# Kernel tuning notes

Measured on AMD Instinct MI355X. Metric: run time of the kernel, lower is better.

## Reference

```python
import jax, jax.numpy as jnp
import numpy as np

N, X_DIM, Y_DIM, HID = 8192, 512, 2048 // 4, 2048
Y_DIM = 512

def setup_inputs() -> dict:
    key = jax.random.key(0)
    ks = jax.random.split(key, 10)
    def lin(k, fan_in, fan_out):
        lim = 1.0 / np.sqrt(fan_in)
        kw, kb = jax.random.split(k)
        W = jax.random.uniform(kw, (fan_in, fan_out), jnp.float32, -lim, lim)
        b = jax.random.uniform(kb, (fan_out,), jnp.float32, -lim, lim)
        return W, b
    mu_W1, mu_b1 = lin(ks[0], X_DIM, HID)
    mu_W2, mu_b2 = lin(ks[1], HID, Y_DIM)
    lv_W1, lv_b1 = lin(ks[2], X_DIM, HID)
    lv_W2, lv_b2 = lin(ks[3], HID, Y_DIM)
    return {
        "x_samples": jax.random.normal(ks[4], (N, X_DIM), jnp.float32),
        "y_samples": jax.random.normal(ks[5], (N, Y_DIM), jnp.float32),
        "mu_W1": mu_W1, "mu_b1": mu_b1, "mu_W2": mu_W2, "mu_b2": mu_b2,
        "lv_W1": lv_W1, "lv_b1": lv_b1, "lv_W2": lv_W2, "lv_b2": lv_b2,
    }

def reference(x_samples, y_samples, mu_W1, mu_b1, mu_W2, mu_b2, lv_W1, lv_b1, lv_W2, lv_b2):
    # MLP heads (GEMMs)
    mu = jax.nn.relu(x_samples @ mu_W1 + mu_b1) @ mu_W2 + mu_b2          # [N, D]
    logvar = jnp.tanh(jax.nn.relu(x_samples @ lv_W1 + lv_b1) @ lv_W2 + lv_b2)  # [N, D]
    w = 0.5 * jnp.exp(-logvar)                                           # 1/(2*exp(logvar))
    n = x_samples.shape[0]

    # positive: -mean_i sum_d (mu_id - y_id)^2 * w_id
    positive = -(((mu - y_samples) ** 2) * w).sum(axis=1).mean()

    # negative (exact decomposition of the [N,N,D] broadcast):
    # -(1/N^2) sum_{i,d} w_id * (N*mu_id^2 - 2*mu_id*Sy_d + Sy2_d)
    Sy = y_samples.sum(axis=0)          # [D]
    Sy2 = (y_samples ** 2).sum(axis=0)  # [D]
    negative = -(w * (n * mu ** 2 - 2.0 * mu * Sy + Sy2)).sum() / (n * n)

    return positive - negative
```

## Files before the change

kernel.cpp:

```cpp
#include <hip/hip_runtime.h>
#include <hip/hip_bf16.h>
#include <stdint.h>

#define NS   8192
#define XD   512
#define HD   2048
#define YD   512

typedef unsigned short u16;
using bf16x8 = __attribute__((ext_vector_type(8))) short;
using f32x4  = __attribute__((ext_vector_type(4))) float;

__device__ __forceinline__ float bf2f(u16 u) {
  union { uint32_t i; float f; } v; v.i = ((uint32_t)u) << 16; return v.f;
}
__device__ __forceinline__ u16 f2b(float f) {
  __hip_bfloat16 hb = __float2bfloat16(f);
  return *(const u16*)&hb;
}
__device__ __forceinline__ float ld_in(const void* p, int f32, size_t i) {
  return f32 ? ((const float*)p)[i] : bf2f(((const u16*)p)[i]);
}
#define GLDS(gp, lp) __builtin_amdgcn_global_load_lds( \
    (__attribute__((address_space(1))) void*)(gp),     \
    (__attribute__((address_space(3))) void*)(lp), 16, 0, 0)

__device__ __forceinline__ int probe_f32(const void* p, int n_u16, int* sflag) {
  if (threadIdx.x == 0) *sflag = 0;
  __syncthreads();
  const u16* q = (const u16*)p;
  int wild = 0;
  for (int i = threadIdx.x; i < n_u16; i += blockDim.x) {
    float v = bf2f(q[i]);
    if (!(fabsf(v) <= 1000.0f)) wild = 1;
  }
  if (wild) *sflag = 1;
  __syncthreads();
  int r = *sflag;
  __syncthreads();
  return r;
}

__device__ __forceinline__ void transpose64(const void* in, u16* out,
                                            int R, int C, int f, int t,
                                            u16* tile ) {
  const int tid = threadIdx.x;
  const int nbx = C >> 6;
  const int c0 = (t % nbx) * 64, r0 = (t / nbx) * 64;
  const int r = tid >> 2, cc = (tid & 3) * 16;
  if (f) {
    const float4* s = (const float4*)((const float*)in + (size_t)(r0 + r) * C + c0 + cc);
#pragma unroll
    for (int k = 0; k < 4; ++k) {
      float4 v = s[k];
      tile[r * 72 + cc + k * 4 + 0] = f2b(v.x);
      tile[r * 72 + cc + k * 4 + 1] = f2b(v.y);
      tile[r * 72 + cc + k * 4 + 2] = f2b(v.z);
      tile[r * 72 + cc + k * 4 + 3] = f2b(v.w);
    }
  } else {
    const uint4* s = (const uint4*)((const u16*)in + (size_t)(r0 + r) * C + c0 + cc);
    *(uint4*)&tile[r * 72 + cc]     = s[0];
    *(uint4*)&tile[r * 72 + cc + 8] = s[1];
  }
  __syncthreads();
  const int i = tid >> 2, jc = (tid & 3) * 16;
  alignas(16) u16 o[16];
#pragma unroll
  for (int j = 0; j < 16; ++j) o[j] = tile[(jc + j) * 72 + i];
  uint4* dq = (uint4*)&out[(size_t)(c0 + i) * R + r0 + jc];
  dq[0] = ((const uint4*)o)[0];
  dq[1] = ((const uint4*)o)[1];
}

__global__ __launch_bounds__(256) void prep_all(
    const void* __restrict__ x, const void* __restrict__ y,
    const void* w1m, const void* b1m, const void* w2m, const void* b2m,
    const void* w1l, const void* b1l, const void* w2l, const void* b2l,
    u16* __restrict__ xb, float* __restrict__ biasv,
    float* __restrict__ Sy, float* __restrict__ Sy2,
    u16* __restrict__ W1t, u16* __restrict__ W2tm, u16* __restrict__ W2tl,
    double* __restrict__ gacc, unsigned* __restrict__ counter) {
  __shared__ alignas(16) u16 tile[64 * 72];
  __shared__ int sflag;
  const int b = blockIdx.x;
  const int tid = threadIdx.x;

  if (b < 64) {
    const int yf = probe_f32(y, 1024, &sflag);
    const int c0 = b * 8;
    float s[8] = {}, q[8] = {};
    if (yf) {
      const float* fy = (const float*)y + c0;
      for (int r = tid; r < NS; r += 256) {
        const float4 a = *(const float4*)(fy + (size_t)r * YD);
        const float4 c = *(const float4*)(fy + (size_t)r * YD + 4);
        s[0]+=a.x; q[0]+=a.x*a.x; s[1]+=a.y; q[1]+=a.y*a.y;
        s[2]+=a.z; q[2]+=a.z*a.z; s[3]+=a.w; q[3]+=a.w*a.w;
        s[4]+=c.x; q[4]+=c.x*c.x; s[5]+=c.y; q[5]+=c.y*c.y;
        s[6]+=c.z; q[6]+=c.z*c.z; s[7]+=c.w; q[7]+=c.w*c.w;
      }
    } else {
      const u16* hy = (const u16*)y + c0;
      for (int r = tid; r < NS; r += 256) {
        const uint4 t4 = *(const uint4*)(hy + (size_t)r * YD);
        const uint32_t w4[4] = {t4.x, t4.y, t4.z, t4.w};
#pragma unroll
        for (int j = 0; j < 4; ++j) {
          const float v0 = bf2f((u16)(w4[j] & 0xffff));
          const float v1 = bf2f((u16)(w4[j] >> 16));
          s[2*j]   += v0; q[2*j]   += v0 * v0;
          s[2*j+1] += v1; q[2*j+1] += v1 * v1;
        }
      }
    }
    float* red = (float*)tile;
#pragma unroll
    for (int j = 0; j < 8; ++j) red[j * 256 + tid] = s[j];
    __syncthreads();
    for (int st = 128; st > 0; st >>= 1) {
      if (tid < st)
#pragma unroll
        for (int j = 0; j < 8; ++j) red[j * 256 + tid] += red[j * 256 + tid + st];
      __syncthreads();
    }
    if (tid < 8) Sy[c0 + tid] = red[tid * 256];
    __syncthreads();
#pragma unroll
    for (int j = 0; j < 8; ++j) red[j * 256 + tid] = q[j];
    __syncthreads();
    for (int st = 128; st > 0; st >>= 1) {
      if (tid < st)
#pragma unroll
        for (int j = 0; j < 8; ++j) red[j * 256 + tid] += red[j * 256 + tid + st];
      __syncthreads();
    }
    if (tid < 8) Sy2[c0 + tid] = red[tid * 256];
  } else if (b < 2112) {
    if (!probe_f32(x, 1024, &sflag)) return;
    const size_t base = (size_t)(b - 64) * 2048 + (size_t)tid * 8;
    alignas(16) u16 o[8];
    const float4* s = (const float4*)((const float*)x + base);
    float4 v0 = s[0], v1 = s[1];
    o[0]=f2b(v0.x); o[1]=f2b(v0.y); o[2]=f2b(v0.z); o[3]=f2b(v0.w);
    o[4]=f2b(v1.x); o[5]=f2b(v1.y); o[6]=f2b(v1.z); o[7]=f2b(v1.w);
    *(uint4*)(xb + base) = *(const uint4*)o;
  } else if (b == 2112) {
    if (tid == 0) { *gacc = 0.0; *counter = 0u; }
    const int f3 = probe_f32(b1m, 1024, &sflag);
    const int f5 = probe_f32(b2m, 512, &sflag);
    const int f7 = probe_f32(b1l, 1024, &sflag);
    const int f9 = probe_f32(b2l, 512, &sflag);
    for (int i = tid; i < 5120; i += 256) {
      float v;
      if (i < 2048)      v = ld_in(b1m, f3, i);
      else if (i < 4096) v = ld_in(b1l, f7, i - 2048);
      else if (i < 4608) v = ld_in(b2m, f5, i - 4096);
      else               v = ld_in(b2l, f9, i - 4608);
      biasv[i] = v;
    }
  } else {
    const int id = b - 2113, which = id >> 8, t = id & 255;
    const void* in; u16* out; int R, C;
    if (which == 0)      { in = w1m; out = W1t;                   R = XD; C = HD; }
    else if (which == 1) { in = w2m; out = W2tm;                  R = HD; C = YD; }
    else if (which == 2) { in = w1l; out = W1t + (size_t)HD * XD; R = XD; C = HD; }
    else                 { in = w2l; out = W2tl;                  R = HD; C = YD; }
    const int f = probe_f32(in, 1024, &sflag);
    transpose64(in, out, R, C, f, t, tile);
  }
}

__global__ __launch_bounds__(256) void gemm1_kernel(
    const void* __restrict__ xraw, const u16* __restrict__ xb,
    const u16* __restrict__ W1t,
    const float* __restrict__ bias,
    u16* __restrict__ h_mu, u16* __restrict__ h_lv) {
  constexpr int K = XD;
  __shared__ alignas(16) u16 As[128 * 64];
  __shared__ alignas(16) u16 Bs[128 * 64];
  __shared__ int sflag;

  const u16* A = probe_f32(xraw, 1024, &sflag) ? xb : (const u16*)xraw;

  const int tid = threadIdx.x, wid = tid >> 6, lane = tid & 63;
  const int MT = NS / 128, NT = (2 * HD) / 128;
  const int id = blockIdx.x;
  const int xcd = id & 7, slot = id >> 3;
  const int bm0 = (xcd * (MT >> 3) + slot / NT) * 128;
  const int bn0 = (slot % NT) * 128;

  const int mrow = (wid >> 1) * 64, ncol = (wid & 1) * 64;
  const int quad = lane >> 4, c16 = lane & 15, cswz = c16 & 7;
  const int srow = lane >> 3, sc = lane & 7;
  const int scg  = (sc ^ srow) * 8;

  f32x4 acc[4][4] = {};

  for (int k0 = 0; k0 < K; k0 += 64) {
#pragma unroll
    for (int j = 0; j < 4; ++j) {
      const int grp = wid * 4 + j, row = grp * 8 + srow;
      GLDS(A   + (size_t)(bm0 + row) * K + (k0 + scg), As + grp * 512);
      GLDS(W1t + (size_t)(bn0 + row) * K + (k0 + scg), Bs + grp * 512);
    }
    __syncthreads();
#pragma unroll
    for (int h = 0; h < 2; ++h) {
      const int off = ((h * 4 + quad) ^ cswz) * 8;
      bf16x8 af[4], bfr[4];
#pragma unroll
      for (int mi = 0; mi < 4; ++mi)
        af[mi] = *(const bf16x8*)&As[(mrow + mi * 16 + c16) * 64 + off];
#pragma unroll
      for (int ni = 0; ni < 4; ++ni)
        bfr[ni] = *(const bf16x8*)&Bs[(ncol + ni * 16 + c16) * 64 + off];
#pragma unroll
      for (int mi = 0; mi < 4; ++mi)
#pragma unroll
        for (int ni = 0; ni < 4; ++ni)
          acc[mi][ni] = __builtin_amdgcn_mfma_f32_16x16x32_bf16(
              af[mi], bfr[ni], acc[mi][ni], 0, 0, 0);
    }
    __syncthreads();
  }

  const bool is_lv = bn0 >= HD;
  u16* dst = is_lv ? h_lv : h_mu;
  const int cb = bn0 - (is_lv ? HD : 0);
#pragma unroll
  for (int ni = 0; ni < 4; ++ni) {
    const int gc = ncol + ni * 16 + c16;
    const float bv = bias[bn0 + gc];
#pragma unroll
    for (int mi = 0; mi < 4; ++mi)
#pragma unroll
      for (int r = 0; r < 4; ++r) {
        const int grow = bm0 + mrow + mi * 16 + quad * 4 + r;
        dst[(size_t)grow * HD + (cb + gc)] = f2b(fmaxf(acc[mi][ni][r] + bv, 0.f));
      }
  }
}

__global__ __launch_bounds__(256) void gemm2_dual(
    const u16* __restrict__ hm, const u16* __restrict__ hl,
    const u16* __restrict__ W2m, const u16* __restrict__ W2l,
    const float* __restrict__ b2m, const float* __restrict__ b2l,
    const void* __restrict__ y,
    const float* __restrict__ Sy, const float* __restrict__ Sy2,
    double* __restrict__ gacc, unsigned* __restrict__ counter,
    float* __restrict__ out) {
  constexpr int K = HD;
  __shared__ alignas(16) u16 Am[64 * 64];
  __shared__ alignas(16) u16 Al[64 * 64];
  __shared__ alignas(16) u16 Bm[128 * 64];
  __shared__ alignas(16) u16 Bl[128 * 64];
  __shared__ double bs[4];
  __shared__ int sflag;

  const int yf = probe_f32(y, 1024, &sflag);

  const int tid = threadIdx.x, wid = tid >> 6, lane = tid & 63;
  const int MT = NS / 64, NT = YD / 128;
  const int id = blockIdx.x;
  const int xcd = id & 7, slot = id >> 3;
  const int bm0 = (xcd * (MT >> 3) + slot / NT) * 64;
  const int bn0 = (slot % NT) * 128;

  const int mrow = (wid >> 1) * 32, ncol = (wid & 1) * 64;
  const int quad = lane >> 4, c16 = lane & 15, cswz = c16 & 7;
  const int srow = lane >> 3, sc = lane & 7;
  const int scg  = (sc ^ srow) * 8;

  f32x4 am[2][4] = {}, al[2][4] = {};

  for (int k0 = 0; k0 < K; k0 += 64) {
#pragma unroll
    for (int j = 0; j < 2; ++j) {
      const int grp = wid * 2 + j, row = grp * 8 + srow;
      const size_t go = (size_t)(bm0 + row) * K + (k0 + scg);
      GLDS(hm + go, Am + grp * 512);
      GLDS(hl + go, Al + grp * 512);
    }
#pragma unroll
    for (int j = 0; j < 4; ++j) {
      const int grp = wid * 4 + j, row = grp * 8 + srow;
      const size_t go = (size_t)(bn0 + row) * K + (k0 + scg);
      GLDS(W2m + go, Bm + grp * 512);
      GLDS(W2l + go, Bl + grp * 512);
    }
    __syncthreads();
#pragma unroll
    for (int h = 0; h < 2; ++h) {
      const int off = ((h * 4 + quad) ^ cswz) * 8;
      bf16x8 afm[2], afl[2], bfm[4], bfl[4];
#pragma unroll
      for (int mi = 0; mi < 2; ++mi) {
        const int rl = (mrow + mi * 16 + c16) * 64 + off;
        afm[mi] = *(const bf16x8*)&Am[rl];
        afl[mi] = *(const bf16x8*)&Al[rl];
      }
#pragma unroll
      for (int ni = 0; ni < 4; ++ni) {
        const int rl = (ncol + ni * 16 + c16) * 64 + off;
        bfm[ni] = *(const bf16x8*)&Bm[rl];
        bfl[ni] = *(const bf16x8*)&Bl[rl];
      }
#pragma unroll
      for (int mi = 0; mi < 2; ++mi)
#pragma unroll
        for (int ni = 0; ni < 4; ++ni) {
          am[mi][ni] = __builtin_amdgcn_mfma_f32_16x16x32_bf16(
              afm[mi], bfm[ni], am[mi][ni], 0, 0, 0);
          al[mi][ni] = __builtin_amdgcn_mfma_f32_16x16x32_bf16(
              afl[mi], bfl[ni], al[mi][ni], 0, 0, 0);
        }
    }
    __syncthreads();
  }

  const float invN = 1.0f / (float)NS;
  float s = 0.f;
#pragma unroll
  for (int ni = 0; ni < 4; ++ni) {
    const int gcol = bn0 + ncol + ni * 16 + c16;
    const float bmv = b2m[gcol], blv = b2l[gcol];
    const float syv = Sy[gcol], sy2v = Sy2[gcol];
#pragma unroll
    for (int mi = 0; mi < 2; ++mi)
#pragma unroll
      for (int r = 0; r < 4; ++r) {
        const int grow = bm0 + mrow + mi * 16 + quad * 4 + r;
        const float m   = am[mi][ni][r] + bmv;
        const float lvp = al[mi][ni][r] + blv;
        const float w   = 0.5f * expf(-tanhf(lvp));
        const float yv  = ld_in(y, yf, (size_t)grow * YD + gcol);
        s += w * (yv * yv - 2.f * m * yv + (2.f * m * syv - sy2v) * invN);
      }
  }
  for (int off = 32; off > 0; off >>= 1) s += __shfl_down(s, off);
  if (lane == 0) bs[wid] = (double)s;
  __syncthreads();
  if (tid == 0) {
    atomicAdd(gacc, bs[0] + bs[1] + bs[2] + bs[3]);
    __threadfence();
    const unsigned old = atomicAdd(counter, 1u);
    if (old == 511u) {
      const double g = atomicAdd(gacc, 0.0);
      out[0] = (float)(-g / (double)NS);
    }
  }
}

extern "C" void kernel_launch(void* const* d_in, const int* in_sizes, int n_in,
                              void* d_out, int out_size, void* d_ws, size_t ws_size,
                              hipStream_t stream) {
  char* ws = (char*)d_ws;
  double*   gacc    = (double*)ws;
  unsigned* counter = (unsigned*)(ws + 8);
  float*    Sy      = (float*)(ws + 128);
  float*    Sy2     = (float*)(ws + 2176);
  float*    biasv   = (float*)(ws + 4224);
  u16* xb   = (u16*)(ws + 24704);
  u16* W1t  = xb + (size_t)NS * XD;
  u16* W2tm = W1t + (size_t)2 * HD * XD;
  u16* W2tl = W2tm + (size_t)YD * HD;
  u16* h_mu = W2tl + (size_t)YD * HD;
  u16* h_lv = h_mu + (size_t)NS * HD;

  prep_all<<<3137, 256, 0, stream>>>(
      d_in[0], d_in[1], d_in[2], d_in[3], d_in[4], d_in[5],
      d_in[6], d_in[7], d_in[8], d_in[9],
      xb, biasv, Sy, Sy2, W1t, W2tm, W2tl, gacc, counter);

  const float* b1  = biasv;
  const float* b2m = biasv + 4096, *b2l = biasv + 4608;

  gemm1_kernel<<<(NS / 128) * ((2 * HD) / 128), 256, 0, stream>>>(
      d_in[0], xb, W1t, b1, h_mu, h_lv);

  gemm2_dual<<<(NS / 64) * (YD / 128), 256, 0, stream>>>(
      h_mu, h_lv, W2tm, W2tl, b2m, b2l, d_in[1], Sy, Sy2,
      gacc, counter, (float*)d_out);
}
```

Measured before the change: 232.2 us.

## Fuse prep and both GEMMs into one persistent cooperative kernel with grid syncs

Replaces the three kernel launches (prep, GEMM1, dual GEMM2) with a single cooperative persistent kernel. Blocks loop over work items and are separated by grid-wide syncs. It also moves all dtype probing to the kernel start and drops the completion counter in favour of a final grid sync. This is meant to remove launch gaps and tail effects between stages. In exchange, the grid size depends on occupancy, so the GEMM stages run with fewer resident blocks and the tile order changes. Every block also re-probes all ten inputs, and grid.sync adds its own cost.

```diff
diff --git a/kernel.cpp b/kernel.cpp
--- a/kernel.cpp
+++ b/kernel.cpp
@@ -1,6 +1,9 @@
 #include <hip/hip_runtime.h>
 #include <hip/hip_bf16.h>
+#include <hip/hip_cooperative_groups.h>
 #include <stdint.h>
+
+namespace cg = cooperative_groups;
 
 #define NS   8192
 #define XD   512
@@ -43,7 +46,7 @@
 
 __device__ __forceinline__ void transpose64(const void* in, u16* out,
                                             int R, int C, int f, int t,
-                                            u16* tile ) {
+                                            u16* tile) {
   const int tid = threadIdx.x;
   const int nbx = C >> 6;
   const int c0 = (t % nbx) * 64, r0 = (t / nbx) * 64;
@@ -73,294 +76,284 @@
   dq[1] = ((const uint4*)o)[1];
 }
 
-__global__ __launch_bounds__(256) void prep_all(
+__global__ __launch_bounds__(256, 3) void fused_all(
     const void* __restrict__ x, const void* __restrict__ y,
-    const void* w1m, const void* b1m, const void* w2m, const void* b2m,
-    const void* w1l, const void* b1l, const void* w2l, const void* b2l,
+    const void* __restrict__ w1m, const void* __restrict__ b1m,
+    const void* __restrict__ w2m, const void* __restrict__ b2m,
+    const void* __restrict__ w1l, const void* __restrict__ b1l,
+    const void* __restrict__ w2l, const void* __restrict__ b2l,
     u16* __restrict__ xb, float* __restrict__ biasv,
     float* __restrict__ Sy, float* __restrict__ Sy2,
     u16* __restrict__ W1t, u16* __restrict__ W2tm, u16* __restrict__ W2tl,
-    double* __restrict__ gacc, unsigned* __restrict__ counter) {
-  __shared__ alignas(16) u16 tile[64 * 72];
+    u16* __restrict__ h_mu, u16* __restrict__ h_lv,
+    double* __restrict__ gacc, float* __restrict__ out) {
+  __shared__ alignas(16) u16 smem[24576];
+  __shared__ double bs[4];
   __shared__ int sflag;
-  const int b = blockIdx.x;
   const int tid = threadIdx.x;
-
-  if (b < 64) {
-    const int yf = probe_f32(y, 1024, &sflag);
-    const int c0 = b * 8;
-    float s[8] = {}, q[8] = {};
-    if (yf) {
-      const float* fy = (const float*)y + c0;
-      for (int r = tid; r < NS; r += 256) {
-        const float4 a = *(const float4*)(fy + (size_t)r * YD);
-        const float4 c = *(const float4*)(fy + (size_t)r * YD + 4);
-        s[0]+=a.x; q[0]+=a.x*a.x; s[1]+=a.y; q[1]+=a.y*a.y;
-        s[2]+=a.z; q[2]+=a.z*a.z; s[3]+=a.w; q[3]+=a.w*a.w;
-        s[4]+=c.x; q[4]+=c.x*c.x; s[5]+=c.y; q[5]+=c.y*c.y;
-        s[6]+=c.z; q[6]+=c.z*c.z; s[7]+=c.w; q[7]+=c.w*c.w;
+  const int bid = blockIdx.x;
+  const int nblk = gridDim.x;
+
+  const int xf   = probe_f32(x,   1024, &sflag);
+  const int yf   = probe_f32(y,   1024, &sflag);
+  const int fw1m = probe_f32(w1m, 1024, &sflag);
+  const int fw2m = probe_f32(w2m, 1024, &sflag);
+  const int fw1l = probe_f32(w1l, 1024, &sflag);
+  const int fw2l = probe_f32(w2l, 1024, &sflag);
+  const int fb1m = probe_f32(b1m, 1024, &sflag);
+  const int fb2m = probe_f32(b2m, 512,  &sflag);
+  const int fb1l = probe_f32(b1l, 1024, &sflag);
+  const int fb2l = probe_f32(b2l, 512,  &sflag);
+
+  for (int w = bid; w < 3137; w += nblk) {
+    if (w < 64) {
+      const int c0 = w * 8;
+      float s[8] = {}, q[8] = {};
+      if (yf) {
+        const float* fy = (const float*)y + c0;
+        for (int r = tid; r < NS; r += 256) {
+          const float4 a = *(const float4*)(fy + (size_t)r * YD);
+          const float4 c = *(const float4*)(fy + (size_t)r * YD + 4);
+          s[0]+=a.x; q[0]+=a.x*a.x; s[1]+=a.y; q[1]+=a.y*a.y;
+          s[2]+=a.z; q[2]+=a.z*a.z; s[3]+=a.w; q[3]+=a.w*a.w;
+          s[4]+=c.x; q[4]+=c.x*c.x; s[5]+=c.y; q[5]+=c.y*c.y;
+          s[6]+=c.z; q[6]+=c.z*c.z; s[7]+=c.w; q[7]+=c.w*c.w;
+        }
+      } else {
+        const u16* hy = (const u16*)y + c0;
+        for (int r = tid; r < NS; r += 256) {
+          const uint4 t4 = *(const uint4*)(hy + (size_t)r * YD);
+          const uint32_t w4[4] = {t4.x, t4.y, t4.z, t4.w};
+#pragma unroll
+          for (int j = 0; j < 4; ++j) {
+            const float v0 = bf2f((u16)(w4[j] & 0xffff));
+            const float v1 = bf2f((u16)(w4[j] >> 16));
+            s[2*j]   += v0; q[2*j]   += v0 * v0;
+            s[2*j+1] += v1; q[2*j+1] += v1 * v1;
+          }
+        }
+      }
+      float* red = (float*)smem;
+#pragma unroll
+      for (int j = 0; j < 8; ++j) red[j * 256 + tid] = s[j];
+      __syncthreads();
+      for (int st = 128; st > 0; st >>= 1) {
+        if (tid < st)
+#pragma unroll
+          for (int j = 0; j < 8; ++j) red[j * 256 + tid] += red[j * 256 + tid + st];
+        __syncthreads();
+      }
+      if (tid < 8) Sy[c0 + tid] = red[tid * 256];
+      __syncthreads();
+#pragma unroll
+      for (int j = 0; j < 8; ++j) red[j * 256 + tid] = q[j];
+      __syncthreads();
+      for (int st = 128; st > 0; st >>= 1) {
+        if (tid < st)
+#pragma unroll
+          for (int j = 0; j < 8; ++j) red[j * 256 + tid] += red[j * 256 + tid + st];
+        __syncthreads();
+      }
+      if (tid < 8) Sy2[c0 + tid] = red[tid * 256];
+    } else if (w < 2112) {
+      if (xf) {
+        const size_t base = (size_t)(w - 64) * 2048 + (size_t)tid * 8;
+        alignas(16) u16 o[8];
+        const float4* s = (const float4*)((const float*)x + base);
+        float4 v0 = s[0], v1 = s[1];
+        o[0]=f2b(v0.x); o[1]=f2b(v0.y); o[2]=f2b(v0.z); o[3]=f2b(v0.w);
+        o[4]=f2b(v1.x); o[5]=f2b(v1.y); o[6]=f2b(v1.z); o[7]=f2b(v1.w);
+        *(uint4*)(xb + base) = *(const uint4*)o;
+      }
+    } else if (w == 2112) {
+      if (tid == 0) *gacc = 0.0;
+      for (int i = tid; i < 5120; i += 256) {
+        float v;
+        if (i < 2048)      v = ld_in(b1m, fb1m, i);
+        else if (i < 4096) v = ld_in(b1l, fb1l, i - 2048);
+        else if (i < 4608) v = ld_in(b2m, fb2m, i - 4096);
+        else               v = ld_in(b2l, fb2l, i - 4608);
+        biasv[i] = v;
       }
     } else {
-      const u16* hy = (const u16*)y + c0;
-      for (int r = tid; r < NS; r += 256) {
-        const uint4 t4 = *(const uint4*)(hy + (size_t)r * YD);
-        const uint32_t w4[4] = {t4.x, t4.y, t4.z, t4.w};
-#pragma unroll
-        for (int j = 0; j < 4; ++j) {
-          const float v0 = bf2f((u16)(w4[j] & 0xffff));
-          const float v1 = bf2f((u16)(w4[j] >> 16));
-          s[2*j]   += v0; q[2*j]   += v0 * v0;
-          s[2*j+1] += v1; q[2*j+1] += v1 * v1;
-        }
-      }
-    }
-    float* red = (float*)tile;
-#pragma unroll
-    for (int j = 0; j < 8; ++j) red[j * 256 + tid] = s[j];
-    __syncthreads();
-    for (int st = 128; st > 0; st >>= 1) {
-      if (tid < st)
-#pragma unroll
-        for (int j = 0; j < 8; ++j) red[j * 256 + tid] += red[j * 256 + tid + st];
-      __syncthreads();
-    }
-    if (tid < 8) Sy[c0 + tid] = red[tid * 256];
-    __syncthreads();
-#pragma unroll
-    for (int j = 0; j < 8; ++j) red[j * 256 + tid] = q[j];
-    __syncthreads();
-    for (int st = 128; st > 0; st >>= 1) {
-      if (tid < st)
-#pragma unroll
-        for (int j = 0; j < 8; ++j) red[j * 256 + tid] += red[j * 256 + tid + st];
-      __syncthreads();
-    }
-    if (tid < 8) Sy2[c0 + tid] = red[tid * 256];
-  } else if (b < 2112) {
-    if (!probe_f32(x, 1024, &sflag)) return;
-    const size_t base = (size_t)(b - 64) * 2048 + (size_t)tid * 8;
-    alignas(16) u16 o[8];
-    const float4* s = (const float4*)((const float*)x + base);
-    float4 v0 = s[0], v1 = s[1];
-    o[0]=f2b(v0.x); o[1]=f2b(v0.y); o[2]=f2b(v0.z); o[3]=f2b(v0.w);
-    o[4]=f2b(v1.x); o[5]=f2b(v1.y); o[6]=f2b(v1.z); o[7]=f2b(v1.w);
-    *(uint4*)(xb + base) = *(const uint4*)o;
-  } else if (b == 2112) {
-    if (tid == 0) { *gacc = 0.0; *counter = 0u; }
-    const int f3 = probe_f32(b1m, 1024, &sflag);
-    const int f5 = probe_f32(b2m, 512, &sflag);
-    const int f7 = probe_f32(b1l, 1024, &sflag);
-    const int f9 = probe_f32(b2l, 512, &sflag);
-    for (int i = tid; i < 5120; i += 256) {
-      float v;
-      if (i < 2048)      v = ld_in(b1m, f3, i);
-      else if (i < 4096) v = ld_in(b1l, f7, i - 2048);
-      else if (i < 4608) v = ld_in(b2m, f5, i - 4096);
-      else               v = ld_in(b2l, f9, i - 4608);
-      biasv[i] = v;
-    }
-  } else {
-    const int id = b - 2113, which = id >> 8, t = id & 255;
-    const void* in; u16* out; int R, C;
-    if (which == 0)      { in = w1m; out = W1t;                   R = XD; C = HD; }
-    else if (which == 1) { in = w2m; out = W2tm;                  R = HD; C = YD; }
-    else if (which == 2) { in = w1l; out = W1t + (size_t)HD * XD; R = XD; C = HD; }
-    else                 { in = w2l; out = W2tl;                  R = HD; C = YD; }
-    const int f = probe_f32(in, 1024, &sflag);
-    transpose64(in, out, R, C, f, t, tile);
-  }
-}
-
-__global__ __launch_bounds__(256) void gemm1_kernel(
-    const void* __restrict__ xraw, const u16* __restrict__ xb,
-    const u16* __restrict__ W1t,
-    const float* __restrict__ bias,
-    u16* __restrict__ h_mu, u16* __restrict__ h_lv) {
-  constexpr int K = XD;
-  __shared__ alignas(16) u16 As[128 * 64];
-  __shared__ alignas(16) u16 Bs[128 * 64];
-  __shared__ int sflag;
-
-  const u16* A = probe_f32(xraw, 1024, &sflag) ? xb : (const u16*)xraw;
-
-  const int tid = threadIdx.x, wid = tid >> 6, lane = tid & 63;
-  const int MT = NS / 128, NT = (2 * HD) / 128;
-  const int id = blockIdx.x;
-  const int xcd = id & 7, slot = id >> 3;
-  const int bm0 = (xcd * (MT >> 3) + slot / NT) * 128;
-  const int bn0 = (slot % NT) * 128;
-
-  const int mrow = (wid >> 1) * 64, ncol = (wid & 1) * 64;
-  const int quad = lane >> 4, c16 = lane & 15, cswz = c16 & 7;
-  const int srow = lane >> 3, sc = lane & 7;
-  const int scg  = (sc ^ srow) * 8;
-
-  f32x4 acc[4][4] = {};
-
-  for (int k0 = 0; k0 < K; k0 += 64) {
-#pragma unroll
-    for (int j = 0; j < 4; ++j) {
-      const int grp = wid * 4 + j, row = grp * 8 + srow;
-      GLDS(A   + (size_t)(bm0 + row) * K + (k0 + scg), As + grp * 512);
-      GLDS(W1t + (size_t)(bn0 + row) * K + (k0 + scg), Bs + grp * 512);
+      const int id = w - 2113, which = id >> 8, t = id & 255;
+      const void* in; u16* out2; int R, C, f;
+      if (which == 0)      { in = w1m; out2 = W1t;                   R = XD; C = HD; f = fw1m; }
+      else if (which == 1) { in = w2m; out2 = W2tm;                  R = HD; C = YD; f = fw2m; }
+      else if (which == 2) { in = w1l; out2 = W1t + (size_t)HD * XD; R = XD; C = HD; f = fw1l; }
+      else                 { in = w2l; out2 = W2tl;                  R = HD; C = YD; f = fw2l; }
+      transpose64(in, out2, R, C, f, t, smem);
     }
     __syncthreads();
-#pragma unroll
-    for (int h = 0; h < 2; ++h) {
-      const int off = ((h * 4 + quad) ^ cswz) * 8;
-      bf16x8 af[4], bfr[4];
-#pragma unroll
-      for (int mi = 0; mi < 4; ++mi)
-        af[mi] = *(const bf16x8*)&As[(mrow + mi * 16 + c16) * 64 + off];
-#pragma unroll
-      for (int ni = 0; ni < 4; ++ni)
-        bfr[ni] = *(const bf16x8*)&Bs[(ncol + ni * 16 + c16) * 64 + off];
-#pragma unroll
-      for (int mi = 0; mi < 4; ++mi)
-#pragma unroll
-        for (int ni = 0; ni < 4; ++ni)
-          acc[mi][ni] = __builtin_amdgcn_mfma_f32_16x16x32_bf16(
-              af[mi], bfr[ni], acc[mi][ni], 0, 0, 0);
+  }
+  cg::this_grid().sync();
+
+  {
+    const u16* A = xf ? xb : (const u16*)x;
+    u16* As = smem;
+    u16* Bs = smem + 8192;
+    const int wid = tid >> 6, lane = tid & 63;
+    const int quad = lane >> 4, c16 = lane & 15, cswz = c16 & 7;
+    const int srow = lane >> 3, sc = lane & 7;
+    const int scg  = (sc ^ srow) * 8;
+    const int mrow = (wid >> 1) * 64, ncol = (wid & 1) * 64;
+
+    for (int t = bid; t < 2048; t += nblk) {
+      const int xcd = t & 7, slot = t >> 3;
+      const int bm0 = (xcd * 8 + slot / 32) * 128;
+      const int bn0 = (slot % 32) * 128;
+      f32x4 acc[4][4] = {};
+
+      for (int k0 = 0; k0 < XD; k0 += 64) {
+#pragma unroll
+        for (int j = 0; j < 4; ++j) {
+          const int grp = wid * 4 + j, row = grp * 8 + srow;
+          GLDS(A   + (size_t)(bm0 + row) * XD + (k0 + scg), As + grp * 512);
+          GLDS(W1t + (size_t)(bn0 + row) * XD + (k0 + scg), Bs + grp * 512);
+        }
+        __syncthreads();
+#pragma unroll
+        for (int h = 0; h < 2; ++h) {
+          const int off = ((h * 4 + quad) ^ cswz) * 8;
+          bf16x8 af[4], bfr[4];
+#pragma unroll
+          for (int mi = 0; mi < 4; ++mi)
+            af[mi] = *(const bf16x8*)&As[(mrow + mi * 16 + c16) * 64 + off];
+#pragma unroll
+          for (int ni = 0; ni < 4; ++ni)
+            bfr[ni] = *(const bf16x8*)&Bs[(ncol + ni * 16 + c16) * 64 + off];
+#pragma unroll
+          for (int mi = 0; mi < 4; ++mi)
+#pragma unroll
+            for (int ni = 0; ni < 4; ++ni)
+              acc[mi][ni] = __builtin_amdgcn_mfma_f32_16x16x32_bf16(
+                  af[mi], bfr[ni], acc[mi][ni], 0, 0, 0);
+        }
+        __syncthreads();
+      }
+
+      const bool is_lv = bn0 >= HD;
+      u16* dst = is_lv ? h_lv : h_mu;
+      const int cb = bn0 - (is_lv ? HD : 0);
+#pragma unroll
+      for (int ni = 0; ni < 4; ++ni) {
+        const int gc = ncol + ni * 16 + c16;
+        const float bv = biasv[bn0 + gc];
+#pragma unroll
+        for (int mi = 0; mi < 4; ++mi)
+#pragma unroll
+          for (int r = 0; r < 4; ++r) {
+            const int grow = bm0 + mrow + mi * 16 + quad * 4 + r;
+            dst[(size_t)grow * HD + (cb + gc)] = f2b(fmaxf(acc[mi][ni][r] + bv, 0.f));
+          }
+      }
     }
-    __syncthreads();
-  }
-
-  const bool is_lv = bn0 >= HD;
-  u16* dst = is_lv ? h_lv : h_mu;
-  const int cb = bn0 - (is_lv ? HD : 0);
-#pragma unroll
-  for (int ni = 0; ni < 4; ++ni) {
-    const int gc = ncol + ni * 16 + c16;
-    const float bv = bias[bn0 + gc];
-#pragma unroll
-    for (int mi = 0; mi < 4; ++mi)
-#pragma unroll
-      for (int r = 0; r < 4; ++r) {
-        const int grow = bm0 + mrow + mi * 16 + quad * 4 + r;
-        dst[(size_t)grow * HD + (cb + gc)] = f2b(fmaxf(acc[mi][ni][r] + bv, 0.f));
-      }
-  }
-}
-
-__global__ __launch_bounds__(256) void gemm2_dual(
-    const u16* __restrict__ hm, const u16* __restrict__ hl,
-    const u16* __restrict__ W2m, const u16* __restrict__ W2l,
-    const float* __restrict__ b2m, const float* __restrict__ b2l,
-    const void* __restrict__ y,
-    const float* __restrict__ Sy, const float* __restrict__ Sy2,
-    double* __restrict__ gacc, unsigned* __restrict__ counter,
-    float* __restrict__ out) {
-  constexpr int K = HD;
-  __shared__ alignas(16) u16 Am[64 * 64];
-  __shared__ alignas(16) u16 Al[64 * 64];
-  __shared__ alignas(16) u16 Bm[128 * 64];
-  __shared__ alignas(16) u16 Bl[128 * 64];
-  __shared__ double bs[4];
-  __shared__ int sflag;
-
-  const int yf = probe_f32(y, 1024, &sflag);
-
-  const int tid = threadIdx.x, wid = tid >> 6, lane = tid & 63;
-  const int MT = NS / 64, NT = YD / 128;
-  const int id = blockIdx.x;
-  const int xcd = id & 7, slot = id >> 3;
-  const int bm0 = (xcd * (MT >> 3) + slot / NT) * 64;
-  const int bn0 = (slot % NT) * 128;
-
-  const int mrow = (wid >> 1) * 32, ncol = (wid & 1) * 64;
-  const int quad = lane >> 4, c16 = lane & 15, cswz = c16 & 7;
-  const int srow = lane >> 3, sc = lane & 7;
-  const int scg  = (sc ^ srow) * 8;
-
-  f32x4 am[2][4] = {}, al[2][4] = {};
-
-  for (int k0 = 0; k0 < K; k0 += 64) {
-#pragma unroll
-    for (int j = 0; j < 2; ++j) {
-      const int grp = wid * 2 + j, row = grp * 8 + srow;
-      const size_t go = (size_t)(bm0 + row) * K + (k0 + scg);
-      GLDS(hm + go, Am + grp * 512);
-      GLDS(hl + go, Al + grp * 512);
+  }
+  cg::this_grid().sync();
+
+  {
+    const float* b2mv = biasv + 4096;
+    const float* b2lv = biasv + 4608;
+    u16* Am = smem;
+    u16* Al = smem + 4096;
+    u16* Bm = smem + 8192;
+    u16* Bl = smem + 16384;
+    const int wid = tid >> 6, lane = tid & 63;
+    const int quad = lane >> 4, c16 = lane & 15, cswz = c16 & 7;
+    const int srow = lane >> 3, sc = lane & 7;
+    const int scg  = (sc ^ srow) * 8;
+    const int mrow = (wid >> 1) * 32, ncol = (wid & 1) * 64;
+    const float invN = 1.0f / (float)NS;
+
+    for (int t = bid; t < 512; t += nblk) {
+      const int xcd = t & 7, slot = t >> 3;
+      const int bm0 = (xcd * 16 + slot / 4) * 64;
+      const int bn0 = (slot % 4) * 128;
+      f32x4 am[2][4] = {}, al[2][4] = {};
+
+      for (int k0 = 0; k0 < HD; k0 += 64) {
+#pragma unroll
+        for (int j = 0; j < 2; ++j) {
+          const int grp = wid * 2 + j, row = grp * 8 + srow;
+          const size_t go = (size_t)(bm0 + row) * HD + (k0 + scg);
+          GLDS(h_mu + go, Am + grp * 512);
+          GLDS(h_lv + go, Al + grp * 512);
+        }
+#pragma unroll
+        for (int j = 0; j < 4; ++j) {
+          const int grp = wid * 4 + j, row = grp * 8 + srow;
+          const size_t go = (size_t)(bn0 + row) * HD + (k0 + scg);
+          GLDS(W2tm + go, Bm + grp * 512);
+          GLDS(W2tl + go, Bl + grp * 512);
+        }
+        __syncthreads();
+#pragma unroll
+        for (int h = 0; h < 2; ++h) {
+          const int off = ((h * 4 + quad) ^ cswz) * 8;
+          bf16x8 afm[2], afl[2], bfm[4], bfl[4];
+#pragma unroll
+          for (int mi = 0; mi < 2; ++mi) {
+            const int rl = (mrow + mi * 16 + c16) * 64 + off;
+            afm[mi] = *(const bf16x8*)&Am[rl];
+            afl[mi] = *(const bf16x8*)&Al[rl];
+          }
+#pragma unroll
+          for (int ni = 0; ni < 4; ++ni) {
+            const int rl = (ncol + ni * 16 + c16) * 64 + off;
+            bfm[ni] = *(const bf16x8*)&Bm[rl];
+            bfl[ni] = *(const bf16x8*)&Bl[rl];
+          }
+#pragma unroll
+          for (int mi = 0; mi < 2; ++mi)
+#pragma unroll
+            for (int ni = 0; ni < 4; ++ni) {
+              am[mi][ni] = __builtin_amdgcn_mfma_f32_16x16x32_bf16(
+                  afm[mi], bfm[ni], am[mi][ni], 0, 0, 0);
+              al[mi][ni] = __builtin_amdgcn_mfma_f32_16x16x32_bf16(
+                  afl[mi], bfl[ni], al[mi][ni], 0, 0, 0);
+            }
+        }
+        __syncthreads();
+      }
+
+      float s = 0.f;
+#pragma unroll
+      for (int ni = 0; ni < 4; ++ni) {
+        const int gcol = bn0 + ncol + ni * 16 + c16;
+        const float bmv = b2mv[gcol], blv = b2lv[gcol];
+        const float syv = Sy[gcol], sy2v = Sy2[gcol];
+#pragma unroll
+        for (int mi = 0; mi < 2; ++mi)
+#pragma unroll
+          for (int r = 0; r < 4; ++r) {
+            const int grow = bm0 + mrow + mi * 16 + quad * 4 + r;
+            const float m   = am[mi][ni][r] + bmv;
+            const float lvp = al[mi][ni][r] + blv;
+            const float wq  = 0.5f * expf(-tanhf(lvp));
+            const float yv  = ld_in(y, yf, (size_t)grow * YD + gcol);
+            s += wq * (yv * yv - 2.f * m * yv + (2.f * m * syv - sy2v) * invN);
+          }
+      }
+      for (int off = 32; off > 0; off >>= 1) s += __shfl_down(s, off);
+      if (lane == 0) bs[wid] = (double)s;
+      __syncthreads();
+      if (tid == 0) atomicAdd(gacc, bs[0] + bs[1] + bs[2] + bs[3]);
+      __syncthreads();
     }
-#pragma unroll
-    for (int j = 0; j < 4; ++j) {
-      const int grp = wid * 4 + j, row = grp * 8 + srow;
-      const size_t go = (size_t)(bn0 + row) * K + (k0 + scg);
-      GLDS(W2m + go, Bm + grp * 512);
-      GLDS(W2l + go, Bl + grp * 512);
-    }
-    __syncthreads();
-#pragma unroll
-    for (int h = 0; h < 2; ++h) {
-      const int off = ((h * 4 + quad) ^ cswz) * 8;
-      bf16x8 afm[2], afl[2], bfm[4], bfl[4];
-#pragma unroll
-      for (int mi = 0; mi < 2; ++mi) {
-        const int rl = (mrow + mi * 16 + c16) * 64 + off;
-        afm[mi] = *(const bf16x8*)&Am[rl];
-        afl[mi] = *(const bf16x8*)&Al[rl];
-      }
-#pragma unroll
-      for (int ni = 0; ni < 4; ++ni) {
-        const int rl = (ncol + ni * 16 + c16) * 64 + off;
-        bfm[ni] = *(const bf16x8*)&Bm[rl];
-        bfl[ni] = *(const bf16x8*)&Bl[rl];
-      }
-#pragma unroll
-      for (int mi = 0; mi < 2; ++mi)
-#pragma unroll
-        for (int ni = 0; ni < 4; ++ni) {
-          am[mi][ni] = __builtin_amdgcn_mfma_f32_16x16x32_bf16(
-              afm[mi], bfm[ni], am[mi][ni], 0, 0, 0);
-          al[mi][ni] = __builtin_amdgcn_mfma_f32_16x16x32_bf16(
-              afl[mi], bfl[ni], al[mi][ni], 0, 0, 0);
-        }
-    }
-    __syncthreads();
-  }
-
-  const float invN = 1.0f / (float)NS;
-  float s = 0.f;
-#pragma unroll
-  for (int ni = 0; ni < 4; ++ni) {
-    const int gcol = bn0 + ncol + ni * 16 + c16;
-    const float bmv = b2m[gcol], blv = b2l[gcol];
-    const float syv = Sy[gcol], sy2v = Sy2[gcol];
-#pragma unroll
-    for (int mi = 0; mi < 2; ++mi)
-#pragma unroll
-      for (int r = 0; r < 4; ++r) {
-        const int grow = bm0 + mrow + mi * 16 + quad * 4 + r;
-        const float m   = am[mi][ni][r] + bmv;
-        const float lvp = al[mi][ni][r] + blv;
-        const float w   = 0.5f * expf(-tanhf(lvp));
-        const float yv  = ld_in(y, yf, (size_t)grow * YD + gcol);
-        s += w * (yv * yv - 2.f * m * yv + (2.f * m * syv - sy2v) * invN);
-      }
-  }
-  for (int off = 32; off > 0; off >>= 1) s += __shfl_down(s, off);
-  if (lane == 0) bs[wid] = (double)s;
-  __syncthreads();
-  if (tid == 0) {
-    atomicAdd(gacc, bs[0] + bs[1] + bs[2] + bs[3]);
-    __threadfence();
-    const unsigned old = atomicAdd(counter, 1u);
-    if (old == 511u) {
-      const double g = atomicAdd(gacc, 0.0);
-      out[0] = (float)(-g / (double)NS);
-    }
-  }
+  }
+  cg::this_grid().sync();
+  if (bid == 0 && tid == 0)
+    out[0] = (float)(-gacc[0] / (double)NS);
 }
 
 extern "C" void kernel_launch(void* const* d_in, const int* in_sizes, int n_in,
                               void* d_out, int out_size, void* d_ws, size_t ws_size,
                               hipStream_t stream) {
   char* ws = (char*)d_ws;
-  double*   gacc    = (double*)ws;
-  unsigned* counter = (unsigned*)(ws + 8);
-  float*    Sy      = (float*)(ws + 128);
-  float*    Sy2     = (float*)(ws + 2176);
-  float*    biasv   = (float*)(ws + 4224);
+  double* gacc  = (double*)ws;
+  float*  Sy    = (float*)(ws + 128);
+  float*  Sy2   = (float*)(ws + 2176);
+  float*  biasv = (float*)(ws + 4224);
   u16* xb   = (u16*)(ws + 24704);
   u16* W1t  = xb + (size_t)NS * XD;
   u16* W2tm = W1t + (size_t)2 * HD * XD;
@@ -368,18 +361,27 @@
   u16* h_mu = W2tl + (size_t)YD * HD;
   u16* h_lv = h_mu + (size_t)NS * HD;
 
-  prep_all<<<3137, 256, 0, stream>>>(
-      d_in[0], d_in[1], d_in[2], d_in[3], d_in[4], d_in[5],
-      d_in[6], d_in[7], d_in[8], d_in[9],
-      xb, biasv, Sy, Sy2, W1t, W2tm, W2tl, gacc, counter);
-
-  const float* b1  = biasv;
-  const float* b2m = biasv + 4096, *b2l = biasv + 4608;
-
-  gemm1_kernel<<<(NS / 128) * ((2 * HD) / 128), 256, 0, stream>>>(
-      d_in[0], xb, W1t, b1, h_mu, h_lv);
-
-  gemm2_dual<<<(NS / 64) * (YD / 128), 256, 0, stream>>>(
-      h_mu, h_lv, W2tm, W2tl, b2m, b2l, d_in[1], Sy, Sy2,
-      gacc, counter, (float*)d_out);
-}
+  int nb = 0;
+  hipOccupancyMaxActiveBlocksPerMultiprocessor(&nb, fused_all, 256, 0);
+  if (nb < 1) nb = 1;
+  if (nb > 4) nb = 4;
+  dim3 grid((unsigned)nb * 256u);
+
+  const void* x_   = d_in[0]; const void* y_   = d_in[1];
+  const void* w1m_ = d_in[2]; const void* b1m_ = d_in[3];
+  const void* w2m_ = d_in[4]; const void* b2m_ = d_in[5];
+  const void* w1l_ = d_in[6]; const void* b1l_ = d_in[7];
+  const void* w2l_ = d_in[8]; const void* b2l_ = d_in[9];
+  float* out_ = (float*)d_out;
+
+  void* args[] = {
+      (void*)&x_, (void*)&y_,
+      (void*)&w1m_, (void*)&b1m_, (void*)&w2m_, (void*)&b2m_,
+      (void*)&w1l_, (void*)&b1l_, (void*)&w2l_, (void*)&b2l_,
+      (void*)&xb, (void*)&biasv, (void*)&Sy, (void*)&Sy2,
+      (void*)&W1t, (void*)&W2tm, (void*)&W2tl,
+      (void*)&h_mu, (void*)&h_lv,
+      (void*)&gacc, (void*)&out_};
+
+  hipLaunchCooperativeKernel(fused_all, grid, dim3(256), args, 0, stream);
+}
```

Measured after the change: 430.9 us. +85.6%, slower.
